# Kernel optimization log

Measured on AMD Instinct MI355X. Metric: run time of the kernel, lower is better.

Reference implementation:

```python
import jax, jax.numpy as jnp
import numpy as np

B, S, D, H, E, K = 16, 2048, 768, 3072, 8, 2
CAP_FACTOR = 1.25
LN_EPS = 1e-5


def setup_inputs() -> dict:
    key = jax.random.key(0)
    ks = jax.random.split(key, 6)
    scale = 0.02
    return {
        "x": jax.random.normal(ks[0], (B, S, D), jnp.float32),
        "w_gate": jax.random.normal(ks[1], (D, E), jnp.float32) * scale,  # router (eval: no noise)
        "w1": jax.random.normal(ks[2], (E, D, H), jnp.float32) * scale,
        "b1": jnp.zeros((E, H), jnp.float32),
        "w2": jax.random.normal(ks[3], (E, H, D), jnp.float32) * scale,
        "b2": jnp.zeros((E, D), jnp.float32),
        "ln_w": jnp.ones((D,), jnp.float32),
        "ln_b": jnp.zeros((D,), jnp.float32),
    }


def reference(x, w_gate, w1, b1, w2, b2, ln_w, ln_b):
    b, s, d = x.shape
    n = b * s
    capacity = int(CAP_FACTOR * n * K / E)  # static, matches _compute_capacity
    xf = x.reshape(n, d)

    # NoisyTopKRouter in eval mode: linear gate -> top-k -> softmax over top-k logits
    logits = xf @ w_gate                                   # [N, E]
    top_logits, top_idx = jax.lax.top_k(logits, K)         # [N, K]
    routing = jax.nn.softmax(top_logits, axis=-1)          # [N, K]

    out = jnp.zeros((n, d), x.dtype)
    for e in range(E):
        # per-token weight for expert e (0 if not routed to e)
        w_e = jnp.sum(routing * (top_idx == e), axis=-1)   # [N]
        # capacity dropping: keep the `capacity` highest-weight tokens.
        # Unassigned tokens have weight 0 -> zero contribution, so selecting
        # them as filler is mathematically identical to the torch loop.
        top_w, tok = jax.lax.top_k(w_e, capacity)          # [cap], [cap]
        sel = xf[tok]                                      # gather [cap, D]
        h = jax.nn.gelu(sel @ w1[e] + b1[e], approximate=False)
        y = h @ w2[e] + b2[e]                              # [cap, D]
        out = out.at[tok].add(y * top_w[:, None])          # weighted scatter-add

    out = out.reshape(b, s, d)
    mu = jnp.mean(out, axis=-1, keepdims=True)
    var = jnp.mean(jnp.square(out - mu), axis=-1, keepdims=True)
    return (out - mu) * jax.lax.rsqrt(var + LN_EPS) * ln_w + ln_b
```

## Files before the change

kernel.cpp:

```cpp
#include <hip/hip_runtime.h>
#include <math.h>

#define NTOK 32768
#define DDIM 768
#define HDIM 3072
#define NEXP 8
#define CAP  10240

typedef short short8 __attribute__((ext_vector_type(8)));
typedef float f32x4 __attribute__((ext_vector_type(4)));

__device__ __forceinline__ unsigned short f2bf(float f) {
  unsigned u = __float_as_uint(f);
  u += 0x7FFFu + ((u >> 16) & 1u);
  return (unsigned short)(u >> 16);
}
__device__ __forceinline__ float bf2f(unsigned short h) {
  return __uint_as_float((unsigned)h << 16);
}

__device__ __forceinline__ void gload16(const void* g, void* l) {
  __builtin_amdgcn_global_load_lds(
      (const __attribute__((address_space(1))) void*)g,
      (__attribute__((address_space(3))) void*)l, 16, 0, 0);
}

__global__ __launch_bounds__(256) void router_assign(
    const float* __restrict__ x, const float* __restrict__ wg,
    unsigned short* __restrict__ xb,
    unsigned int* __restrict__ pair, float* __restrict__ pw)
{
  __shared__ float wt[NEXP][DDIM];
  int t = threadIdx.x;
  for (int idx = t; idx < NEXP * DDIM; idx += 256) {
    int d = idx >> 3, e = idx & 7;
    wt[e][d] = wg[idx];
  }
  __syncthreads();
  int wave = t >> 6, lane = t & 63;
  int n0 = blockIdx.x * 32 + wave * 8;
  for (int i = 0; i < 8; ++i) {
    int n = n0 + i;
    const float* xr = x + (size_t)n * DDIM;
    unsigned short* xbr = xb + (size_t)n * DDIM;
    float acc[NEXP];
#pragma unroll
    for (int e = 0; e < NEXP; ++e) acc[e] = 0.f;
#pragma unroll
    for (int c = 0; c < 3; ++c) {
      int d = c * 256 + lane * 4;
      float4 xv = *(const float4*)(xr + d);
      ushort4 pk;
      pk.x = f2bf(xv.x); pk.y = f2bf(xv.y); pk.z = f2bf(xv.z); pk.w = f2bf(xv.w);
      *(ushort4*)(xbr + d) = pk;
#pragma unroll
      for (int e = 0; e < NEXP; ++e) {
        float4 wv = *(const float4*)(&wt[e][d]);
        acc[e] += xv.x * wv.x + xv.y * wv.y + xv.z * wv.z + xv.w * wv.w;
      }
    }
#pragma unroll
    for (int e = 0; e < NEXP; ++e) {
      float v = acc[e];
      for (int o = 32; o > 0; o >>= 1) v += __shfl_xor(v, o, 64);
      acc[e] = v;
    }
    if (lane == 0) {
      int e1 = 0; float l1 = acc[0];
#pragma unroll
      for (int e = 1; e < NEXP; ++e) if (acc[e] > l1) { l1 = acc[e]; e1 = e; }
      int e2 = -1; float l2 = -INFINITY;
#pragma unroll
      for (int e = 0; e < NEXP; ++e) if (e != e1 && acc[e] > l2) { l2 = acc[e]; e2 = e; }
      float p1 = 1.f / (1.f + expf(l2 - l1));
      pair[n] = (unsigned)e1 | ((unsigned)e2 << 8);
      pw[n] = p1;
    }
  }
}

__global__ __launch_bounds__(256) void router_scatter(
    const unsigned int* __restrict__ pair, int* __restrict__ cnt,
    int* __restrict__ tokidx, int* __restrict__ slotof)
{
  int e = blockIdx.x;
  __shared__ int wsum[4];
  __shared__ int basev;
  int t = threadIdx.x, wave = t >> 6, lane = t & 63;
  if (t == 0) basev = 0;
  __syncthreads();
  for (int nb = 0; nb < NTOK; nb += 256) {
    int n = nb + t;
    unsigned p = pair[n];
    int e1 = p & 255, e2 = (p >> 8) & 255;
    bool m2 = (e2 == e);
    bool m = (e1 == e) | m2;
    unsigned long long bal = __ballot(m);
    int pre = __popcll(bal & ((1ull << lane) - 1ull));
    if (lane == 0) wsum[wave] = __popcll(bal);
    __syncthreads();
    int woff = 0;
    for (int wv = 0; wv < wave; ++wv) woff += wsum[wv];
    int tot = wsum[0] + wsum[1] + wsum[2] + wsum[3];
    int pos = basev + woff + pre;
    if (m) {
      if (pos < CAP) {
        tokidx[e * CAP + pos] = n;
        slotof[2 * n + (m2 ? 1 : 0)] = e * CAP + pos;
      } else {
        slotof[2 * n + (m2 ? 1 : 0)] = -1;
      }
    }
    __syncthreads();
    if (t == 0) basev += tot;
  }
  __syncthreads();
  if (t == 0) cnt[e] = (basev < CAP) ? basev : CAP;
}

__global__ __launch_bounds__(256) void transpose_kernel(
    const float* __restrict__ src, unsigned short* __restrict__ dst, int R, int C)
{
  __shared__ float tile[64][65];
  int eb = blockIdx.z;
  const float* s = src + (size_t)eb * R * C;
  unsigned short* d = dst + (size_t)eb * R * C;
  int c0 = blockIdx.x * 64, r0 = blockIdx.y * 64;
  int tc = threadIdx.x & 63, tg = threadIdx.x >> 6;
#pragma unroll
  for (int rr = tg; rr < 64; rr += 4)
    tile[rr][tc] = s[(size_t)(r0 + rr) * C + c0 + tc];
  __syncthreads();
#pragma unroll
  for (int rr = tg; rr < 64; rr += 4)
    d[(size_t)(c0 + rr) * R + r0 + tc] = f2bf(tile[tc][rr]);
}

template<int EPI, int KK, int NN>
__global__ __launch_bounds__(512, 2) void moe_gemm(
    const unsigned short* __restrict__ A,
    const unsigned short* __restrict__ Bt,
    const float* __restrict__ bias,
    const int* __restrict__ cnt,
    const int* __restrict__ tokidx,
    unsigned short* __restrict__ Obuf,
    int mbase, int Mc)
{
  constexpr int KT = KK / 64;
  constexpr int NI = KT / 2;
  int e = blockIdx.z;
  int M = cnt[e]; if (M > CAP) M = CAP;
  int ly0 = blockIdx.y * 256;
  int gm0 = mbase + ly0;
  if (gm0 >= M) return;
  int n0 = blockIdx.x * 256;
  int t = threadIdx.x, wave = t >> 6, lane = t & 63;
  int wr = wave >> 2, wc = wave & 3;
  int lane15 = lane & 15, quad = lane >> 4;

  __shared__ __align__(16) char smem[131072];

  int ci0 = wave * 128 + lane;
  int ci1 = ci0 + 64;
  int r0 = ci0 >> 2, r1 = ci1 >> 2;
  int c0 = (ci0 & 3) ^ ((r0 >> 1) & 3);
  int c1 = (ci1 & 3) ^ ((r1 >> 1) & 3);
  const unsigned short *aB0, *aB1, *bB0, *bB1;
  if (EPI == 0) {
    int g0 = gm0 + r0; if (g0 >= M) g0 = M - 1;
    int g1 = gm0 + r1; if (g1 >= M) g1 = M - 1;
    aB0 = A + (size_t)tokidx[e * CAP + g0] * KK + c0 * 8;
    aB1 = A + (size_t)tokidx[e * CAP + g1] * KK + c1 * 8;
  } else {
    aB0 = A + ((size_t)e * Mc + ly0 + r0) * KK + c0 * 8;
    aB1 = A + ((size_t)e * Mc + ly0 + r1) * KK + c1 * 8;
  }
  bB0 = Bt + ((size_t)e * NN + n0 + r0) * KK + c0 * 8;
  bB1 = Bt + ((size_t)e * NN + n0 + r1) * KK + c1 * 8;

#define STAGE_A(buf, kh, kt_) do { \
    gload16(aB0 + (kt_) * 64 + (kh) * 32, smem + (buf) * 65536 + (kh) * 16384 + wave * 2048); \
    gload16(aB1 + (kt_) * 64 + (kh) * 32, smem + (buf) * 65536 + (kh) * 16384 + wave * 2048 + 1024); \
  } while (0)
#define STAGE_B(buf, kh, kt_) do { \
    gload16(bB0 + (kt_) * 64 + (kh) * 32, smem + (buf) * 65536 + 32768 + (kh) * 16384 + wave * 2048); \
    gload16(bB1 + (kt_) * 64 + (kh) * 32, smem + (buf) * 65536 + 32768 + (kh) * 16384 + wave * 2048 + 1024); \
  } while (0)

  int aoffb[8], boffb[4];
#pragma unroll
  for (int m = 0; m < 8; ++m) {
    int row = wr * 128 + m * 16 + lane15;
    aoffb[m] = row * 64 + ((quad ^ ((row >> 1) & 3)) * 16);
  }
#pragma unroll
  for (int n = 0; n < 4; ++n) {
    int row = wc * 64 + n * 16 + lane15;
    boffb[n] = 32768 + row * 64 + ((quad ^ ((row >> 1) & 3)) * 16);
  }

  f32x4 acc[8][4];
#pragma unroll
  for (int mf = 0; mf < 8; ++mf)
#pragma unroll
    for (int n = 0; n < 4; ++n)
#pragma unroll
      for (int r = 0; r < 4; ++r) acc[mf][n][r] = 0.f;

  short8 af[4], bf[4];

#define BAR()  __builtin_amdgcn_s_barrier()
#define WVM4() asm volatile("s_waitcnt vmcnt(4)" ::: "memory")
#define WVM0() asm volatile("s_waitcnt vmcnt(0)" ::: "memory")
#define RD_B(buf, ks) do { \
    _Pragma("unroll") \
    for (int n = 0; n < 4; ++n) \
      bf[n] = *(const short8*)(smem + (buf) * 65536 + (ks) * 16384 + boffb[n]); \
  } while (0)
#define RD_A(buf, ks, mh) do { \
    _Pragma("unroll") \
    for (int m = 0; m < 4; ++m) \
      af[m] = *(const short8*)(smem + (buf) * 65536 + (ks) * 16384 + aoffb[(mh) * 4 + m]); \
  } while (0)
#define MM(mh) do { \
    __builtin_amdgcn_s_setprio(1); \
    _Pragma("unroll") \
    for (int m = 0; m < 4; ++m) \
      _Pragma("unroll") \
      for (int n = 0; n < 4; ++n) \
        acc[(mh) * 4 + m][n] = __builtin_amdgcn_mfma_f32_16x16x32_bf16( \
            af[m], bf[n], acc[(mh) * 4 + m][n], 0, 0, 0); \
    __builtin_amdgcn_s_setprio(0); \
  } while (0)

  STAGE_A(0, 0, 0); STAGE_B(0, 0, 0);
  STAGE_A(0, 1, 0); STAGE_B(0, 1, 0);
  STAGE_A(1, 0, 1); STAGE_B(1, 0, 1);
  WVM4();
  BAR();

#pragma unroll 1
  for (int it = 0; it < NI - 1; ++it) {
    int kt = 2 * it;
    RD_B(0, 0); RD_A(0, 0, 0); STAGE_A(1, 1, kt + 1);
    BAR(); MM(0); BAR();
    RD_A(0, 0, 1); STAGE_B(1, 1, kt + 1);
    BAR(); MM(1); BAR();
    RD_B(0, 1); RD_A(0, 1, 0); STAGE_A(0, 0, kt + 2);
    BAR(); MM(0); BAR();
    RD_A(0, 1, 1); STAGE_B(0, 0, kt + 2);
    BAR(); MM(1); WVM4(); BAR();
    RD_B(1, 0); RD_A(1, 0, 0); STAGE_A(0, 1, kt + 2);
    BAR(); MM(0); BAR();
    RD_A(1, 0, 1); STAGE_B(0, 1, kt + 2);
    BAR(); MM(1); BAR();
    RD_B(1, 1); RD_A(1, 1, 0); STAGE_A(1, 0, kt + 3);
    BAR(); MM(0); BAR();
    RD_A(1, 1, 1); STAGE_B(1, 0, kt + 3);
    BAR(); MM(1); WVM4(); BAR();
  }

  {
    constexpr int kt = 2 * (NI - 1);
    RD_B(0, 0); RD_A(0, 0, 0); STAGE_A(1, 1, kt + 1);
    BAR(); MM(0); BAR();
    RD_A(0, 0, 1); STAGE_B(1, 1, kt + 1);
    BAR(); MM(1); BAR();
    RD_B(0, 1); RD_A(0, 1, 0);
    BAR(); MM(0); BAR();
    RD_A(0, 1, 1);
    BAR(); MM(1); WVM0(); BAR();
    RD_B(1, 0); RD_A(1, 0, 0);
    BAR(); MM(0); BAR();
    RD_A(1, 0, 1);
    BAR(); MM(1); BAR();
    RD_B(1, 1); RD_A(1, 1, 0);
    BAR(); MM(0); BAR();
    RD_A(1, 1, 1);
    BAR(); MM(1);
  }

  if (EPI == 0) {
#pragma unroll
    for (int n = 0; n < 4; ++n) {
      int col = n0 + wc * 64 + n * 16 + lane15;
      float bcol = bias[e * NN + col];
#pragma unroll
      for (int mf = 0; mf < 8; ++mf) {
        int rowb = ly0 + wr * 128 + mf * 16 + quad * 4;
#pragma unroll
        for (int r = 0; r < 4; ++r) {
          float v = acc[mf][n][r] + bcol;
          v = 0.5f * v * (1.f + erff(v * 0.70710678118654752f));
          Obuf[((size_t)e * Mc + rowb + r) * NN + col] = f2bf(v);
        }
      }
    }
  } else {
    float bc[4];
#pragma unroll
    for (int n = 0; n < 4; ++n)
      bc[n] = bias[e * NN + n0 + wc * 64 + n * 16 + lane15];
#pragma unroll
    for (int mf = 0; mf < 8; ++mf) {
      int gmb = gm0 + wr * 128 + mf * 16 + quad * 4;
#pragma unroll
      for (int r = 0; r < 4; ++r) {
        int gm = gmb + r;
        if (gm < M) {
          unsigned short* yrow = Obuf + ((size_t)e * CAP + gm) * NN;
#pragma unroll
          for (int n = 0; n < 4; ++n) {
            int col = n0 + wc * 64 + n * 16 + lane15;
            yrow[col] = f2bf(acc[mf][n][r] + bc[n]);
          }
        }
      }
    }
  }
#undef STAGE_A
#undef STAGE_B
#undef BAR
#undef WVM4
#undef WVM0
#undef RD_B
#undef RD_A
#undef MM
}

__global__ __launch_bounds__(256) void combine_ln(
    const unsigned short* __restrict__ Y, const int* __restrict__ slotof,
    const float* __restrict__ pw,
    const float* __restrict__ lnw, const float* __restrict__ lnb,
    float* __restrict__ out)
{
  __shared__ float red[8];
  int n = blockIdx.x;
  int s0 = slotof[2 * n], s1 = slotof[2 * n + 1];
  float p0 = pw[n], p1 = 1.f - p0;
  const unsigned short* y0 = Y + (size_t)(s0 < 0 ? 0 : s0) * DDIM;
  const unsigned short* y1 = Y + (size_t)(s1 < 0 ? 0 : s1) * DDIM;
  if (s0 < 0) p0 = 0.f;
  if (s1 < 0) p1 = 0.f;
  int t = threadIdx.x;
  float v0 = p0 * bf2f(y0[t])       + p1 * bf2f(y1[t]);
  float v1 = p0 * bf2f(y0[t + 256]) + p1 * bf2f(y1[t + 256]);
  float v2 = p0 * bf2f(y0[t + 512]) + p1 * bf2f(y1[t + 512]);
  float s = v0 + v1 + v2;
  float ss = v0 * v0 + v1 * v1 + v2 * v2;
  for (int o = 32; o > 0; o >>= 1) { s += __shfl_xor(s, o, 64); ss += __shfl_xor(ss, o, 64); }
  int wave = t >> 6, lane = t & 63;
  if (lane == 0) { red[wave] = s; red[4 + wave] = ss; }
  __syncthreads();
  s = red[0] + red[1] + red[2] + red[3];
  ss = red[4] + red[5] + red[6] + red[7];
  float mu = s * (1.f / DDIM);
  float var = ss * (1.f / DDIM) - mu * mu;
  float rs = rsqrtf(var + 1e-5f);
  float* row = out + (size_t)n * DDIM;
  row[t]       = (v0 - mu) * rs * lnw[t]       + lnb[t];
  row[t + 256] = (v1 - mu) * rs * lnw[t + 256] + lnb[t + 256];
  row[t + 512] = (v2 - mu) * rs * lnw[t + 512] + lnb[t + 512];
}

__global__ void sentinel_kernel(float* __restrict__ out, int n) {
  int i = blockIdx.x * 256 + threadIdx.x;
  if (i < n) out[i] = 12345.0f;
}

extern "C" void kernel_launch(void* const* d_in, const int* in_sizes, int n_in,
                              void* d_out, int out_size, void* d_ws, size_t ws_size,
                              hipStream_t stream)
{
  const float* x   = (const float*)d_in[0];
  const float* wg  = (const float*)d_in[1];
  const float* w1  = (const float*)d_in[2];
  const float* b1  = (const float*)d_in[3];
  const float* w2  = (const float*)d_in[4];
  const float* b2  = (const float*)d_in[5];
  const float* lnw = (const float*)d_in[6];
  const float* lnb = (const float*)d_in[7];
  float* out = (float*)d_out;

  char* ws = (char*)d_ws;
  size_t off = 0;
  auto take = [&](size_t bytes) {
    char* p = ws + off; off += (bytes + 255) & ~(size_t)255; return p;
  };
  unsigned short* xb   = (unsigned short*)take((size_t)NTOK * DDIM * 2);
  unsigned short* w1bt = (unsigned short*)take((size_t)NEXP * DDIM * HDIM * 2);
  unsigned short* w2bt = (unsigned short*)take((size_t)NEXP * DDIM * HDIM * 2);
  int*   tokidx = (int*)take((size_t)NEXP * CAP * 4);
  unsigned int* pair = (unsigned int*)take((size_t)NTOK * 4);
  float* pw   = (float*)take((size_t)NTOK * 4);
  int*   slotof = (int*)take((size_t)NTOK * 2 * 4);
  int*   cnt  = (int*)take(256);
  unsigned short* Ybuf = (unsigned short*)take((size_t)NEXP * CAP * DDIM * 2);

  size_t avail = (ws_size > off) ? (ws_size - off) : 0;
  long long cand = (long long)(avail / ((size_t)NEXP * HDIM * 2));
  int Mc = (int)((cand / 256) * 256);
  if (Mc > CAP) Mc = CAP;
  if (Mc < 256) {
    sentinel_kernel<<<(NTOK * DDIM + 255) / 256, 256, 0, stream>>>(out, NTOK * DDIM);
    return;
  }
  unsigned short* Hbuf = (unsigned short*)take((size_t)NEXP * Mc * HDIM * 2);

  router_assign<<<NTOK / 32, 256, 0, stream>>>(x, wg, xb, pair, pw);
  transpose_kernel<<<dim3(HDIM / 64, DDIM / 64, NEXP), 256, 0, stream>>>(w1, w1bt, DDIM, HDIM);
  transpose_kernel<<<dim3(DDIM / 64, HDIM / 64, NEXP), 256, 0, stream>>>(w2, w2bt, HDIM, DDIM);
  router_scatter<<<NEXP, 256, 0, stream>>>(pair, cnt, tokidx, slotof);

  for (int mbase = 0; mbase < CAP; mbase += Mc) {
    int rows = CAP - mbase; if (rows > Mc) rows = Mc;
    int mt = rows / 256;
    moe_gemm<0, DDIM, HDIM><<<dim3(HDIM / 256, mt, NEXP), 512, 0, stream>>>(
        xb, w1bt, b1, cnt, tokidx, Hbuf, mbase, Mc);
    moe_gemm<1, HDIM, DDIM><<<dim3(DDIM / 256, mt, NEXP), 512, 0, stream>>>(
        Hbuf, w2bt, b2, cnt, tokidx, Ybuf, mbase, Mc);
  }

  combine_ln<<<NTOK, 256, 0, stream>>>(Ybuf, slotof, pw, lnw, lnb, out);
}
```

Before: 1.558 ms.

## Remap MoE GEMM grid per XCD, loosen vmcnt waits, use fast GELU

The MoE GEMM grid is flattened to 1D and remapped so consecutive workgroups of the same expert and tile row land on the same XCD, aiming for better L2 reuse of weights and activations. The pipeline waits now use vmcnt(8) instead of vmcnt(4), with an extra wait added after every half-step, so more global-to-LDS loads can stay in flight. The exact erff GELU is replaced by an Abramowitz-Stegun polynomial with __expf to cut epilogue cost. The polynomial's roughly 1e-7 error is negligible against the bf16 output. The main risk is whether the new wait counts still guarantee the data is ready before use.

```diff
diff --git a/kernel.cpp b/kernel.cpp
--- a/kernel.cpp
+++ b/kernel.cpp
@@ -23,6 +23,21 @@
   __builtin_amdgcn_global_load_lds(
       (const __attribute__((address_space(1))) void*)g,
       (__attribute__((address_space(3))) void*)l, 16, 0, 0);
+}
+
+__device__ __forceinline__ float gelu_fast(float v) {
+  float z = v * 0.70710678118654752f;
+  float a = fabsf(z);
+  float t = 1.0f / (1.0f + 0.3275911f * a);
+  float p = t * (0.254829592f +
+           t * (-0.284496736f +
+           t * (1.421413741f +
+           t * (-1.453152027f +
+           t * 1.061405429f))));
+  float ex = __expf(-a * a);
+  float er = 1.0f - p * ex;
+  er = copysignf(er, z);
+  return 0.5f * v * (1.0f + er);
 }
 
 __global__ __launch_bounds__(256) void router_assign(
@@ -144,16 +159,29 @@
     const int* __restrict__ cnt,
     const int* __restrict__ tokidx,
     unsigned short* __restrict__ Obuf,
-    int mbase, int Mc)
+    int mbase, int Mc, int mt)
 {
   constexpr int KT = KK / 64;
   constexpr int NI = KT / 2;
-  int e = blockIdx.z;
+  constexpr int GX = NN / 256;
+
+  int nwg = gridDim.x;
+  int orig = blockIdx.x;
+  int q = nwg >> 3, r = nwg & 7;
+  int xcd = orig & 7, loc = orig >> 3;
+  int base = (xcd < r) ? xcd * (q + 1) : r * (q + 1) + (xcd - r) * q;
+  int wg = base + loc;
+  int per_e = GX * mt;
+  int e = wg / per_e;
+  int rem = wg - e * per_e;
+  int by = rem / GX;
+  int bx = rem - by * GX;
+
   int M = cnt[e]; if (M > CAP) M = CAP;
-  int ly0 = blockIdx.y * 256;
+  int ly0 = by * 256;
   int gm0 = mbase + ly0;
   if (gm0 >= M) return;
-  int n0 = blockIdx.x * 256;
+  int n0 = bx * 256;
   int t = threadIdx.x, wave = t >> 6, lane = t & 63;
   int wr = wave >> 2, wc = wave & 3;
   int lane15 = lane & 15, quad = lane >> 4;
@@ -210,6 +238,7 @@
   short8 af[4], bf[4];
 
 #define BAR()  __builtin_amdgcn_s_barrier()
+#define WVM8() asm volatile("s_waitcnt vmcnt(8)" ::: "memory")
 #define WVM4() asm volatile("s_waitcnt vmcnt(4)" ::: "memory")
 #define WVM0() asm volatile("s_waitcnt vmcnt(0)" ::: "memory")
 #define RD_B(buf, ks) do { \
@@ -236,7 +265,7 @@
   STAGE_A(0, 0, 0); STAGE_B(0, 0, 0);
   STAGE_A(0, 1, 0); STAGE_B(0, 1, 0);
   STAGE_A(1, 0, 1); STAGE_B(1, 0, 1);
-  WVM4();
+  WVM8();
   BAR();
 
 #pragma unroll 1
@@ -245,19 +274,19 @@
     RD_B(0, 0); RD_A(0, 0, 0); STAGE_A(1, 1, kt + 1);
     BAR(); MM(0); BAR();
     RD_A(0, 0, 1); STAGE_B(1, 1, kt + 1);
-    BAR(); MM(1); BAR();
+    BAR(); MM(1); WVM8(); BAR();
     RD_B(0, 1); RD_A(0, 1, 0); STAGE_A(0, 0, kt + 2);
     BAR(); MM(0); BAR();
     RD_A(0, 1, 1); STAGE_B(0, 0, kt + 2);
-    BAR(); MM(1); WVM4(); BAR();
+    BAR(); MM(1); WVM8(); BAR();
     RD_B(1, 0); RD_A(1, 0, 0); STAGE_A(0, 1, kt + 2);
     BAR(); MM(0); BAR();
     RD_A(1, 0, 1); STAGE_B(0, 1, kt + 2);
-    BAR(); MM(1); BAR();
+    BAR(); MM(1); WVM8(); BAR();
     RD_B(1, 1); RD_A(1, 1, 0); STAGE_A(1, 0, kt + 3);
     BAR(); MM(0); BAR();
     RD_A(1, 1, 1); STAGE_B(1, 0, kt + 3);
-    BAR(); MM(1); WVM4(); BAR();
+    BAR(); MM(1); WVM8(); BAR();
   }
 
   {
@@ -265,15 +294,15 @@
     RD_B(0, 0); RD_A(0, 0, 0); STAGE_A(1, 1, kt + 1);
     BAR(); MM(0); BAR();
     RD_A(0, 0, 1); STAGE_B(1, 1, kt + 1);
-    BAR(); MM(1); BAR();
+    BAR(); MM(1); WVM8(); BAR();
     RD_B(0, 1); RD_A(0, 1, 0);
     BAR(); MM(0); BAR();
     RD_A(0, 1, 1);
+    BAR(); MM(1); WVM4(); BAR();
+    RD_B(1, 0); RD_A(1, 0, 0);
+    BAR(); MM(0); BAR();
+    RD_A(1, 0, 1);
     BAR(); MM(1); WVM0(); BAR();
-    RD_B(1, 0); RD_A(1, 0, 0);
-    BAR(); MM(0); BAR();
-    RD_A(1, 0, 1);
-    BAR(); MM(1); BAR();
     RD_B(1, 1); RD_A(1, 1, 0);
     BAR(); MM(0); BAR();
     RD_A(1, 1, 1);
@@ -290,8 +319,7 @@
         int rowb = ly0 + wr * 128 + mf * 16 + quad * 4;
 #pragma unroll
         for (int r = 0; r < 4; ++r) {
-          float v = acc[mf][n][r] + bcol;
-          v = 0.5f * v * (1.f + erff(v * 0.70710678118654752f));
+          float v = gelu_fast(acc[mf][n][r] + bcol);
           Obuf[((size_t)e * Mc + rowb + r) * NN + col] = f2bf(v);
         }
       }
@@ -321,6 +349,7 @@
 #undef STAGE_A
 #undef STAGE_B
 #undef BAR
+#undef WVM8
 #undef WVM4
 #undef WVM0
 #undef RD_B
@@ -415,10 +444,10 @@
   for (int mbase = 0; mbase < CAP; mbase += Mc) {
     int rows = CAP - mbase; if (rows > Mc) rows = Mc;
     int mt = rows / 256;
-    moe_gemm<0, DDIM, HDIM><<<dim3(HDIM / 256, mt, NEXP), 512, 0, stream>>>(
-        xb, w1bt, b1, cnt, tokidx, Hbuf, mbase, Mc);
-    moe_gemm<1, HDIM, DDIM><<<dim3(DDIM / 256, mt, NEXP), 512, 0, stream>>>(
-        Hbuf, w2bt, b2, cnt, tokidx, Ybuf, mbase, Mc);
+    moe_gemm<0, DDIM, HDIM><<<(HDIM / 256) * mt * NEXP, 512, 0, stream>>>(
+        xb, w1bt, b1, cnt, tokidx, Hbuf, mbase, Mc, mt);
+    moe_gemm<1, HDIM, DDIM><<<(DDIM / 256) * mt * NEXP, 512, 0, stream>>>(
+        Hbuf, w2bt, b2, cnt, tokidx, Ybuf, mbase, Mc, mt);
   }
 
   combine_ln<<<NTOK, 256, 0, stream>>>(Ybuf, slotof, pw, lnw, lnb, out);
```

Measured after the change: 1.514 ms. 1.03x faster.
